# Kernel tuning notes

Measured on AMD Instinct MI355X. Metric: run time of the kernel, lower is better.

Reference implementation:

```python
import jax, jax.numpy as jnp
import numpy as np

B, S, D = 8, 1024, 1024   # batch, routed-over rows, feature dim (input_dim)
E = 1024                  # output_dim (== S so gather indices are in range)
K = 2                     # top-k
ALPHA = 0.01


def setup_inputs() -> dict:
    key = jax.random.key(0)
    kx, kw = jax.random.split(key)
    x = jax.random.normal(kx, (B, S, D), dtype=jnp.float32)
    # nn.Linear(input_dim, output_dim, bias=False) weight: [E, D]
    W = jax.random.normal(kw, (E, D), dtype=jnp.float32) / np.sqrt(D).astype(np.float32)
    return {"x": x, "W": W}


def reference(x, W):
    # logits = proj(x): [B, S, E]  (temperature == 1.0 -> no scaling)
    logits = jnp.einsum('bsd,ed->bse', x, W)
    probs = jax.nn.softmax(logits, axis=-1)
    topk_probs, topk_idx = jax.lax.top_k(probs, K)            # [B, S, K]
    # router_selections: gather rows of x along dim 1 -> [B, S, K, D]
    sel = x[jnp.arange(B)[:, None, None], topk_idx]
    # y = sum_k topk_probs * selected rows -> [B, S, D]
    y = jnp.einsum('bsk,bskd->bsd', topk_probs, sel)
    # auxiliary load-balance loss
    router_probs = probs.mean(axis=(0, 1))                    # [E]
    counts = jnp.bincount(topk_idx.reshape(-1), length=E).astype(probs.dtype)
    router_fraction = counts / counts.sum()
    aux_loss = ALPHA * E * jnp.sum(router_probs * router_fraction)
    return y, aux_loss
```

## Files before the change

kernel.cpp:

```cpp
#include <hip/hip_runtime.h>

#define MTOK 8192
#define ED   1024

typedef short s16x8 __attribute__((ext_vector_type(8)));
typedef float f32x4 __attribute__((ext_vector_type(4)));
typedef unsigned short u16x4 __attribute__((ext_vector_type(4)));

__device__ __forceinline__ unsigned short f2bf(float f) {
    unsigned u = __builtin_bit_cast(unsigned, f);
    u += 0x7fff + ((u >> 16) & 1);
    return (unsigned short)(u >> 16);
}
__device__ __forceinline__ float bf2f(unsigned short h) {
    unsigned u = ((unsigned)h) << 16;
    return __builtin_bit_cast(float, u);
}

__global__ __launch_bounds__(256) void split_bf16_kernel(
        const float* __restrict__ src, unsigned short* __restrict__ hi,
        unsigned short* __restrict__ lo, int n4) {
    int idx = blockIdx.x * 256 + threadIdx.x;
    const int stride = gridDim.x * 256;
    for (; idx < n4; idx += stride) {
        float4 v = ((const float4*)src)[idx];
        u16x4 h, l;
        h[0] = f2bf(v.x); l[0] = f2bf(v.x - bf2f(h[0]));
        h[1] = f2bf(v.y); l[1] = f2bf(v.y - bf2f(h[1]));
        h[2] = f2bf(v.z); l[2] = f2bf(v.z - bf2f(h[2]));
        h[3] = f2bf(v.w); l[3] = f2bf(v.w - bf2f(h[3]));
        ((u16x4*)hi)[idx] = h;
        ((u16x4*)lo)[idx] = l;
    }
}

__device__ __forceinline__ void gload16(const void* g, void* l) {
    __builtin_amdgcn_global_load_lds(
        (const __attribute__((address_space(1))) void*)g,
        (__attribute__((address_space(3))) void*)l, 16, 0, 0);
}

__global__ __launch_bounds__(256, 2) void gemm_mfma_split_kernel(
        const unsigned short* __restrict__ Xhi, const unsigned short* __restrict__ Xlo,
        const unsigned short* __restrict__ Whi, const unsigned short* __restrict__ Wlo,
        float* __restrict__ C) {
    __shared__ unsigned short smem[2 * 16384];

    const int bid = blockIdx.x;
    const int xcd = bid & 7;
    const int j   = bid >> 3;
    const int bm  = xcd * 8 + (j >> 3);
    const int bn  = j & 7;

    const int tid  = threadIdx.x;
    const int lane = tid & 63;
    const int wid  = tid >> 6;

    const int srow = lane >> 2;
    const int sg   = (lane & 3) ^ ((srow >> 1) & 3);
    const unsigned short* gsrc;
    unsigned short* ldst;
    {
        size_t rb;
        if (wid == 0)      { gsrc = Xhi; ldst = smem;         rb = (size_t)bm * 128; }
        else if (wid == 1) { gsrc = Xlo; ldst = smem + 4096;  rb = (size_t)bm * 128; }
        else if (wid == 2) { gsrc = Whi; ldst = smem + 8192;  rb = (size_t)bn * 128; }
        else               { gsrc = Wlo; ldst = smem + 12288; rb = (size_t)bn * 128; }
        gsrc += (rb + srow) * ED + sg * 8;
    }

#define STAGE(buf, kk)                                                        \
    {                                                                          \
        unsigned short* dst = ldst + (buf) * 16384;                            \
        const unsigned short* src = gsrc + (kk);                               \
        _Pragma("unroll")                                                      \
        for (int c = 0; c < 8; ++c)                                            \
            gload16(src + c * (16 * ED), dst + c * 512);                       \
    }

    const int wm = wid >> 1, wn = wid & 1;
    const int fr = lane & 15, fg = lane >> 4;
    const int pg = fg ^ ((fr >> 1) & 3);
    const int aoff = (wm * 64 + fr) * 32 + pg * 8;
    const int boff = (wn * 64 + fr) * 32 + pg * 8;

    f32x4 acc[4][4] = {};

    STAGE(0, 0);
    asm volatile("s_waitcnt vmcnt(0)" ::: "memory");
    __builtin_amdgcn_s_barrier();

    for (int t = 0; t < 32; ++t) {
        const int cur = t & 1;
        if (t < 31) STAGE(cur ^ 1, (t + 1) * 32);

        const unsigned short* Ah = smem + cur * 16384;
        const unsigned short* Al = Ah + 4096;
        const unsigned short* Bh = Ah + 8192;
        const unsigned short* Bl = Ah + 12288;

        s16x8 ah[4], al[4], bh[4], bl[4];
#pragma unroll
        for (int i = 0; i < 4; ++i) {
            ah[i] = *(const s16x8*)&Ah[aoff + i * 512];
            al[i] = *(const s16x8*)&Al[aoff + i * 512];
            bh[i] = *(const s16x8*)&Bh[boff + i * 512];
            bl[i] = *(const s16x8*)&Bl[boff + i * 512];
        }
#pragma unroll
        for (int i = 0; i < 4; ++i)
#pragma unroll
            for (int jj = 0; jj < 4; ++jj) {
                acc[i][jj] = __builtin_amdgcn_mfma_f32_16x16x32_bf16(ah[i], bh[jj], acc[i][jj], 0, 0, 0);
                acc[i][jj] = __builtin_amdgcn_mfma_f32_16x16x32_bf16(ah[i], bl[jj], acc[i][jj], 0, 0, 0);
                acc[i][jj] = __builtin_amdgcn_mfma_f32_16x16x32_bf16(al[i], bh[jj], acc[i][jj], 0, 0, 0);
            }

        asm volatile("s_waitcnt vmcnt(0)" ::: "memory");
        __builtin_amdgcn_s_barrier();
    }
#undef STAGE

    const int crow = bm * 128 + wm * 64 + fg * 4;
    const int ccol = bn * 128 + wn * 64 + fr;
#pragma unroll
    for (int i = 0; i < 4; ++i)
#pragma unroll
        for (int jj = 0; jj < 4; ++jj)
#pragma unroll
            for (int r = 0; r < 4; ++r)
                C[(size_t)(crow + i * 16 + r) * ED + ccol + jj * 16] = acc[i][jj][r];
}

#define BM 128
#define BN 128
#define BK 32
#define LDA (BM + 4)
#define LDB (BN + 4)

__global__ __launch_bounds__(256) void gemm_logits_kernel(const float* __restrict__ X,
                                                          const float* __restrict__ W,
                                                          float* __restrict__ C) {
    __shared__ float As[BK][LDA];
    __shared__ float Bs[BK][LDB];
    const int bm  = blockIdx.y * BM;
    const int bn  = blockIdx.x * BN;
    const int tid = threadIdx.x;
    const int tx  = tid & 15;
    const int ty  = tid >> 4;
    const int lr  = tid >> 3;
    const int lc  = (tid & 7) << 2;

    float acc[8][8];
#pragma unroll
    for (int i = 0; i < 8; ++i)
#pragma unroll
        for (int j = 0; j < 8; ++j) acc[i][j] = 0.f;

    for (int k0 = 0; k0 < ED; k0 += BK) {
#pragma unroll
        for (int i = 0; i < 4; ++i) {
            const int r = lr + i * 32;
            float4 va = *(const float4*)&X[(size_t)(bm + r) * ED + k0 + lc];
            As[lc + 0][r] = va.x; As[lc + 1][r] = va.y;
            As[lc + 2][r] = va.z; As[lc + 3][r] = va.w;
            float4 vb = *(const float4*)&W[(size_t)(bn + r) * ED + k0 + lc];
            Bs[lc + 0][r] = vb.x; Bs[lc + 1][r] = vb.y;
            Bs[lc + 2][r] = vb.z; Bs[lc + 3][r] = vb.w;
        }
        __syncthreads();
#pragma unroll
        for (int kk = 0; kk < BK; ++kk) {
            float a[8], b[8];
            *(float4*)&a[0] = *(const float4*)&As[kk][ty * 8];
            *(float4*)&a[4] = *(const float4*)&As[kk][ty * 8 + 4];
            *(float4*)&b[0] = *(const float4*)&Bs[kk][tx * 8];
            *(float4*)&b[4] = *(const float4*)&Bs[kk][tx * 8 + 4];
#pragma unroll
            for (int i = 0; i < 8; ++i)
#pragma unroll
                for (int j = 0; j < 8; ++j)
                    acc[i][j] = fmaf(a[i], b[j], acc[i][j]);
        }
        __syncthreads();
    }
#pragma unroll
    for (int i = 0; i < 8; ++i) {
        const int r = bm + ty * 8 + i;
        float4* dst = (float4*)&C[(size_t)r * ED + bn + tx * 8];
        dst[0] = make_float4(acc[i][0], acc[i][1], acc[i][2], acc[i][3]);
        dst[1] = make_float4(acc[i][4], acc[i][5], acc[i][6], acc[i][7]);
    }
}

__device__ __forceinline__ bool better(float v, int i, float bv, int bi) {
    return (v > bv) || (v == bv && i < bi);
}

__global__ __launch_bounds__(256, 8) void softmax_wave_kernel(
        const float* __restrict__ X, float* __restrict__ OUT,
        float* __restrict__ partial, int* __restrict__ counts) {
    __shared__ float L[4 * 1024];
    const int tid  = threadIdx.x;
    const int lane = tid & 63;
    const int w    = tid >> 6;
    const int t    = blockIdx.x * 4 + w;

    const float4* row4 = (const float4*)&OUT[(size_t)t * ED];
    float4 p[4];
#pragma unroll
    for (int i = 0; i < 4; ++i) p[i] = row4[lane + 64 * i];

    float v1 = -1e30f, v2 = -1e30f; int i1 = 0x7fffffff, i2 = 0x7fffffff;
#pragma unroll
    for (int i = 0; i < 4; ++i) {
        const float vv[4] = {p[i].x, p[i].y, p[i].z, p[i].w};
#pragma unroll
        for (int c = 0; c < 4; ++c) {
            const int e = 256 * i + 4 * lane + c;
            const float v = vv[c];
            if (better(v, e, v1, i1)) { v2 = v1; i2 = i1; v1 = v; i1 = e; }
            else if (better(v, e, v2, i2)) { v2 = v; i2 = e; }
        }
    }
#pragma unroll
    for (int off = 32; off; off >>= 1) {
        const float ov1 = __shfl_xor(v1, off); const int oi1 = __shfl_xor(i1, off);
        const float ov2 = __shfl_xor(v2, off); const int oi2 = __shfl_xor(i2, off);
        if (better(ov1, oi1, v1, i1)) {
            float nv2; int ni2;
            if (better(v1, i1, ov2, oi2)) { nv2 = v1; ni2 = i1; }
            else { nv2 = ov2; ni2 = oi2; }
            v1 = ov1; i1 = oi1; v2 = nv2; i2 = ni2;
        } else if (better(ov1, oi1, v2, i2)) { v2 = ov1; i2 = oi1; }
    }
    const float m = v1;

    float s = 0.f;
#pragma unroll
    for (int i = 0; i < 4; ++i) {
        p[i].x = __expf(p[i].x - m); p[i].y = __expf(p[i].y - m);
        p[i].z = __expf(p[i].z - m); p[i].w = __expf(p[i].w - m);
        s += p[i].x + p[i].y + p[i].z + p[i].w;
    }
#pragma unroll
    for (int off = 32; off; off >>= 1) s += __shfl_xor(s, off);
    const float inv = 1.f / s;

#pragma unroll
    for (int i = 0; i < 4; ++i) {
        float4 q = make_float4(p[i].x * inv, p[i].y * inv, p[i].z * inv, p[i].w * inv);
        *(float4*)&L[w * 1024 + i * 256 + lane * 4] = q;
    }

    const float p1 = inv;
    const float p2 = __expf(v2 - m) * inv;
    const int b = t >> 10;
    const float4* x1 = (const float4*)&X[((size_t)(b << 10) + i1) * ED];
    const float4* x2 = (const float4*)&X[((size_t)(b << 10) + i2) * ED];
    float4* yrow = (float4*)&OUT[(size_t)t * ED];
#pragma unroll
    for (int i = 0; i < 4; ++i) {
        const int idx = lane + 64 * i;
        const float4 a = x1[idx];
        const float4 c = x2[idx];
        float4 r;
        r.x = fmaf(p1, a.x, p2 * c.x);
        r.y = fmaf(p1, a.y, p2 * c.y);
        r.z = fmaf(p1, a.z, p2 * c.z);
        r.w = fmaf(p1, a.w, p2 * c.w);
        yrow[idx] = r;
    }

    if (lane == 0) { atomicAdd(&counts[i1], 1); atomicAdd(&counts[i2], 1); }

    __syncthreads();
    float4 s0 = *(float4*)&L[0 * 1024 + tid * 4];
    float4 s1 = *(float4*)&L[1 * 1024 + tid * 4];
    float4 s2 = *(float4*)&L[2 * 1024 + tid * 4];
    float4 s3 = *(float4*)&L[3 * 1024 + tid * 4];
    float4 r;
    r.x = (s0.x + s1.x) + (s2.x + s3.x);
    r.y = (s0.y + s1.y) + (s2.y + s3.y);
    r.z = (s0.z + s1.z) + (s2.z + s3.z);
    r.w = (s0.w + s1.w) + (s2.w + s3.w);
    *(float4*)&partial[(size_t)blockIdx.x * 1024 + tid * 4] = r;
}

__global__ __launch_bounds__(256) void aux1_kernel(const float* __restrict__ partial,
                                                   const int* __restrict__ counts,
                                                   float* __restrict__ dotPartial) {
    __shared__ float red[16][16];
    const int tid = threadIdx.x;
    const int el  = tid & 15;
    const int ch  = tid >> 4;
    const int e   = blockIdx.x * 16 + el;
    float s = 0.f;
    for (int k = 0; k < 128; ++k)
        s += partial[(size_t)(ch * 128 + k) * 1024 + e];
    red[ch][el] = s;
    __syncthreads();
    if (tid < 16) {
        float rs = 0.f;
#pragma unroll
        for (int c = 0; c < 16; ++c) rs += red[c][tid];
        float val = rs * (float)counts[blockIdx.x * 16 + tid];
#pragma unroll
        for (int off = 8; off; off >>= 1) val += __shfl_xor(val, off);
        if (tid == 0) dotPartial[blockIdx.x] = val;
    }
}

__global__ void aux2_kernel(const float* __restrict__ dotPartial, float* __restrict__ out) {
    const int lane = threadIdx.x;
    float v = dotPartial[lane];
#pragma unroll
    for (int off = 32; off; off >>= 1) v += __shfl_xor(v, off);
    if (lane == 0)
        out[(size_t)MTOK * ED] = v * (0.01f * 1024.f / (8192.f * 16384.f));
}

#define TOKS_PER_BLK 16
__global__ __launch_bounds__(256) void softmax_topk_y_kernel(
        const float* __restrict__ X, float* __restrict__ OUT,
        float* __restrict__ router_sum, int* __restrict__ counts) {
    __shared__ float routerLocal[ED];
    __shared__ float redMax[4];
    __shared__ float redSum[4];
    __shared__ float wV1[4]; __shared__ int wI1[4];
    __shared__ float wV2[4]; __shared__ int wI2[4];

    const int tid  = threadIdx.x;
    const int lane = tid & 63;
    const int wave = tid >> 6;

    for (int e = tid; e < ED; e += 256) routerLocal[e] = 0.f;
    __syncthreads();

    const int t0 = blockIdx.x * TOKS_PER_BLK;
    for (int t = t0; t < t0 + TOKS_PER_BLK; ++t) {
        const float* lrow = &OUT[(size_t)t * ED];
        float l[4];
#pragma unroll
        for (int i = 0; i < 4; ++i) l[i] = lrow[tid + i * 256];

        float m = fmaxf(fmaxf(l[0], l[1]), fmaxf(l[2], l[3]));
#pragma unroll
        for (int off = 32; off; off >>= 1) m = fmaxf(m, __shfl_xor(m, off));
        if (lane == 0) redMax[wave] = m;
        __syncthreads();
        m = fmaxf(fmaxf(redMax[0], redMax[1]), fmaxf(redMax[2], redMax[3]));

        float p[4]; float s = 0.f;
#pragma unroll
        for (int i = 0; i < 4; ++i) { p[i] = expf(l[i] - m); s += p[i]; }
#pragma unroll
        for (int off = 32; off; off >>= 1) s += __shfl_xor(s, off);
        if (lane == 0) redSum[wave] = s;

        float v1 = -1e30f, v2 = -1e30f; int i1 = 0x7fffffff, i2 = 0x7fffffff;
#pragma unroll
        for (int i = 0; i < 4; ++i) {
            const float v = l[i]; const int ix = tid + i * 256;
            if (better(v, ix, v1, i1)) { v2 = v1; i2 = i1; v1 = v; i1 = ix; }
            else if (better(v, ix, v2, i2)) { v2 = v; i2 = ix; }
        }
#pragma unroll
        for (int off = 32; off; off >>= 1) {
            const float ov1 = __shfl_xor(v1, off); const int oi1 = __shfl_xor(i1, off);
            const float ov2 = __shfl_xor(v2, off); const int oi2 = __shfl_xor(i2, off);
            if (better(ov1, oi1, v1, i1)) {
                float nv2; int ni2;
                if (better(v1, i1, ov2, oi2)) { nv2 = v1; ni2 = i1; }
                else { nv2 = ov2; ni2 = oi2; }
                v1 = ov1; i1 = oi1; v2 = nv2; i2 = ni2;
            } else if (better(ov1, oi1, v2, i2)) { v2 = ov1; i2 = oi1; }
        }
        if (lane == 0) { wV1[wave] = v1; wI1[wave] = i1; wV2[wave] = v2; wI2[wave] = i2; }
        __syncthreads();

        v1 = wV1[0]; i1 = wI1[0]; v2 = wV2[0]; i2 = wI2[0];
#pragma unroll
        for (int w = 1; w < 4; ++w) {
            const float ov1 = wV1[w]; const int oi1 = wI1[w];
            const float ov2 = wV2[w]; const int oi2 = wI2[w];
            if (better(ov1, oi1, v1, i1)) {
                float nv2; int ni2;
                if (better(v1, i1, ov2, oi2)) { nv2 = v1; ni2 = i1; }
                else { nv2 = ov2; ni2 = oi2; }
                v1 = ov1; i1 = oi1; v2 = nv2; i2 = ni2;
            } else if (better(ov1, oi1, v2, i2)) { v2 = ov1; i2 = oi1; }
        }
        const float stot = redSum[0] + redSum[1] + redSum[2] + redSum[3];
        const float inv = 1.f / stot;

#pragma unroll
        for (int i = 0; i < 4; ++i) routerLocal[tid + i * 256] += p[i] * inv;

        const float p1 = expf(v1 - m) * inv;
        const float p2 = expf(v2 - m) * inv;

        const int b = t >> 10;
        const float4* x1 = (const float4*)&X[((size_t)(b << 10) + i1) * ED];
        const float4* x2 = (const float4*)&X[((size_t)(b << 10) + i2) * ED];
        float4* yrow = (float4*)&OUT[(size_t)t * ED];
        const float4 a = x1[tid];
        const float4 c = x2[tid];
        float4 r;
        r.x = fmaf(p1, a.x, p2 * c.x);
        r.y = fmaf(p1, a.y, p2 * c.y);
        r.z = fmaf(p1, a.z, p2 * c.z);
        r.w = fmaf(p1, a.w, p2 * c.w);
        yrow[tid] = r;

        if (tid == 0) { atomicAdd(&counts[i1], 1); atomicAdd(&counts[i2], 1); }
        __syncthreads();
    }

    for (int e = tid; e < ED; e += 256) atomicAdd(&router_sum[e], routerLocal[e]);
}

__global__ __launch_bounds__(256) void aux_kernel(const float* __restrict__ router_sum,
                                                  const int* __restrict__ counts,
                                                  float* __restrict__ out) {
    __shared__ float red[4];
    const int tid = threadIdx.x;
    float s = 0.f;
    for (int e = tid; e < ED; e += 256)
        s += (router_sum[e] * (1.f / 8192.f)) * ((float)counts[e] * (1.f / 16384.f));
#pragma unroll
    for (int off = 32; off; off >>= 1) s += __shfl_xor(s, off);
    if ((tid & 63) == 0) red[tid >> 6] = s;
    __syncthreads();
    if (tid == 0) out[(size_t)MTOK * ED] = 0.01f * 1024.f * (red[0] + red[1] + red[2] + red[3]);
}

extern "C" void kernel_launch(void* const* d_in, const int* in_sizes, int n_in,
                              void* d_out, int out_size, void* d_ws, size_t ws_size,
                              hipStream_t stream) {
    const float* X = (const float*)d_in[0];
    const float* W = (const float*)d_in[1];
    float* out = (float*)d_out;

    const size_t WS_NEED = (size_t)MTOK * ED * 2 * sizeof(unsigned short)
                         + (size_t)ED * ED * 2 * sizeof(unsigned short)
                         + ED * (sizeof(float) + sizeof(int));

    if (ws_size >= WS_NEED) {
        unsigned short* Xhi = (unsigned short*)d_ws;
        unsigned short* Xlo = Xhi + (size_t)MTOK * ED;
        unsigned short* Whi = Xlo + (size_t)MTOK * ED;
        unsigned short* Wlo = Whi + (size_t)ED * ED;
        float* tail         = (float*)(Wlo + (size_t)ED * ED);
        float* dotPartial   = tail;
        int*   counts       = (int*)(tail + ED);
        float* partial      = (float*)Xlo;

        hipMemsetAsync(counts, 0, ED * sizeof(int), stream);
        split_bf16_kernel<<<2048, 256, 0, stream>>>(X, Xhi, Xlo, MTOK * ED / 4);
        split_bf16_kernel<<<512, 256, 0, stream>>>(W, Whi, Wlo, ED * ED / 4);
        gemm_mfma_split_kernel<<<512, 256, 0, stream>>>(Xhi, Xlo, Whi, Wlo, out);
        softmax_wave_kernel<<<MTOK / 4, 256, 0, stream>>>(X, out, partial, counts);
        aux1_kernel<<<64, 256, 0, stream>>>(partial, counts, dotPartial);
        aux2_kernel<<<1, 64, 0, stream>>>(dotPartial, out);
    } else {
        float* router_sum = (float*)d_ws;
        int*   counts     = (int*)((char*)d_ws + ED * sizeof(float));
        hipMemsetAsync(d_ws, 0, ED * (sizeof(float) + sizeof(int)), stream);
        dim3 ggrid(ED / BN, MTOK / BM);
        gemm_logits_kernel<<<ggrid, 256, 0, stream>>>(X, W, out);
        softmax_topk_y_kernel<<<MTOK / TOKS_PER_BLK, 256, 0, stream>>>(X, out, router_sum, counts);
        aux_kernel<<<1, 256, 0, stream>>>(router_sum, counts, out);
    }
}
```

Measured before the change: 101.2 us.

## Software-pipeline GEMM main loop with register double-buffered LDS fragments

Restructures the split-bf16 GEMM K-loop into a two-stage unrolled pipeline. Fragments for the next tile are read from LDS into a second register set while the MFMAs for the current tile run, and global-to-LDS prefetch stays two tiles deep using partial vmcnt waits instead of draining to zero every iteration. The aim is to hide LDS and global latency behind MFMA work. The cost is doubled fragment registers, which may lower occupancy, and more complex barrier and waitcnt ordering.

```diff
diff --git a/kernel.cpp b/kernel.cpp
--- a/kernel.cpp
+++ b/kernel.cpp
@@ -84,42 +84,62 @@
     const int aoff = (wm * 64 + fr) * 32 + pg * 8;
     const int boff = (wn * 64 + fr) * 32 + pg * 8;
 
+    s16x8 ah0[4], al0[4], bh0[4], bl0[4];
+    s16x8 ah1[4], al1[4], bh1[4], bl1[4];
     f32x4 acc[4][4] = {};
 
+#define READF(S, BUF)                                                         \
+    {                                                                          \
+        const unsigned short* _b = smem + (BUF) * 16384;                       \
+        _Pragma("unroll")                                                      \
+        for (int i = 0; i < 4; ++i) {                                          \
+            ah##S[i] = *(const s16x8*)&_b[aoff + i * 512];                     \
+            al##S[i] = *(const s16x8*)&_b[4096 + aoff + i * 512];              \
+            bh##S[i] = *(const s16x8*)&_b[8192 + boff + i * 512];              \
+            bl##S[i] = *(const s16x8*)&_b[12288 + boff + i * 512];             \
+        }                                                                      \
+    }
+
+#define MFMAC(S)                                                               \
+    _Pragma("unroll")                                                          \
+    for (int i = 0; i < 4; ++i)                                                \
+        _Pragma("unroll")                                                      \
+        for (int jj = 0; jj < 4; ++jj) {                                       \
+            acc[i][jj] = __builtin_amdgcn_mfma_f32_16x16x32_bf16(ah##S[i], bh##S[jj], acc[i][jj], 0, 0, 0); \
+            acc[i][jj] = __builtin_amdgcn_mfma_f32_16x16x32_bf16(ah##S[i], bl##S[jj], acc[i][jj], 0, 0, 0); \
+            acc[i][jj] = __builtin_amdgcn_mfma_f32_16x16x32_bf16(al##S[i], bh##S[jj], acc[i][jj], 0, 0, 0); \
+        }
+
     STAGE(0, 0);
+    STAGE(1, 32);
+    asm volatile("s_waitcnt vmcnt(8)" ::: "memory");
+    __builtin_amdgcn_s_barrier();
+    READF(0, 0);
+
+    for (int t2 = 0; t2 < 30; t2 += 2) {
+        asm volatile("s_waitcnt lgkmcnt(0)" ::: "memory");
+        __builtin_amdgcn_s_barrier();
+        STAGE(0, (t2 + 2) * 32);
+        asm volatile("s_waitcnt vmcnt(8)" ::: "memory");
+        __builtin_amdgcn_s_barrier();
+        READF(1, 1);
+        MFMAC(0);
+        asm volatile("s_waitcnt lgkmcnt(0)" ::: "memory");
+        __builtin_amdgcn_s_barrier();
+        STAGE(1, (t2 + 3) * 32);
+        asm volatile("s_waitcnt vmcnt(8)" ::: "memory");
+        __builtin_amdgcn_s_barrier();
+        READF(0, 0);
+        MFMAC(1);
+    }
     asm volatile("s_waitcnt vmcnt(0)" ::: "memory");
     __builtin_amdgcn_s_barrier();
-
-    for (int t = 0; t < 32; ++t) {
-        const int cur = t & 1;
-        if (t < 31) STAGE(cur ^ 1, (t + 1) * 32);
-
-        const unsigned short* Ah = smem + cur * 16384;
-        const unsigned short* Al = Ah + 4096;
-        const unsigned short* Bh = Ah + 8192;
-        const unsigned short* Bl = Ah + 12288;
-
-        s16x8 ah[4], al[4], bh[4], bl[4];
-#pragma unroll
-        for (int i = 0; i < 4; ++i) {
-            ah[i] = *(const s16x8*)&Ah[aoff + i * 512];
-            al[i] = *(const s16x8*)&Al[aoff + i * 512];
-            bh[i] = *(const s16x8*)&Bh[boff + i * 512];
-            bl[i] = *(const s16x8*)&Bl[boff + i * 512];
-        }
-#pragma unroll
-        for (int i = 0; i < 4; ++i)
-#pragma unroll
-            for (int jj = 0; jj < 4; ++jj) {
-                acc[i][jj] = __builtin_amdgcn_mfma_f32_16x16x32_bf16(ah[i], bh[jj], acc[i][jj], 0, 0, 0);
-                acc[i][jj] = __builtin_amdgcn_mfma_f32_16x16x32_bf16(ah[i], bl[jj], acc[i][jj], 0, 0, 0);
-                acc[i][jj] = __builtin_amdgcn_mfma_f32_16x16x32_bf16(al[i], bh[jj], acc[i][jj], 0, 0, 0);
-            }
-
-        asm volatile("s_waitcnt vmcnt(0)" ::: "memory");
-        __builtin_amdgcn_s_barrier();
-    }
+    READF(1, 1);
+    MFMAC(0);
+    MFMAC(1);
 #undef STAGE
+#undef READF
+#undef MFMAC
 
     const int crow = bm * 128 + wm * 64 + fg * 4;
     const int ccol = bn * 128 + wn * 64 + fr;
```

Result: no change. 100.9 us (-0.3%).

## Fuse X bf16 hi/lo split into GEMM by loading fp32 tiles to LDS

Applied to the files above, without the earlier changes.

Removes the separate pass that splits X (8192x1024 fp32) into bf16 hi/lo arrays. The GEMM now stages fp32 X tiles into LDS with a swizzle and converts them to hi/lo bf16 in registers using v_cvt_pk_bf16_f32 before the MFMAs. This drops a full read and write of the X split buffers and shrinks the workspace. In exchange it doubles the LDS footprint per buffer, moves conversion ALU work into the GEMM inner loop, and adds an lgkmcnt wait. The conversion is redone by each of the 8 column blocks that reads a given X tile.

```diff
diff --git a/kernel.cpp b/kernel.cpp
--- a/kernel.cpp
+++ b/kernel.cpp
@@ -5,6 +5,7 @@
 
 typedef short s16x8 __attribute__((ext_vector_type(8)));
 typedef float f32x4 __attribute__((ext_vector_type(4)));
+typedef int   i32x4 __attribute__((ext_vector_type(4)));
 typedef unsigned short u16x4 __attribute__((ext_vector_type(4)));
 
 __device__ __forceinline__ unsigned short f2bf(float f) {
@@ -40,11 +41,17 @@
         (__attribute__((address_space(3))) void*)l, 16, 0, 0);
 }
 
+__device__ __forceinline__ int cvtpk(float a, float b) {
+    int r;
+    asm("v_cvt_pk_bf16_f32 %0, %1, %2" : "=v"(r) : "v"(a), "v"(b));
+    return r;
+}
+
 __global__ __launch_bounds__(256, 2) void gemm_mfma_split_kernel(
-        const unsigned short* __restrict__ Xhi, const unsigned short* __restrict__ Xlo,
+        const float* __restrict__ Xf,
         const unsigned short* __restrict__ Whi, const unsigned short* __restrict__ Wlo,
         float* __restrict__ C) {
-    __shared__ unsigned short smem[2 * 16384];
+    __shared__ __align__(16) unsigned char smem[2 * 32768];
 
     const int bid = blockIdx.x;
     const int xcd = bid & 7;
@@ -56,33 +63,33 @@
     const int lane = tid & 63;
     const int wid  = tid >> 6;
 
+    const float* gsrcF = Xf + (size_t)(bm * 128 + wid * 64 + (lane >> 3)) * ED
+                            + (((lane & 7) ^ (lane >> 3)) << 2);
     const int srow = lane >> 2;
     const int sg   = (lane & 3) ^ ((srow >> 1) & 3);
-    const unsigned short* gsrc;
-    unsigned short* ldst;
-    {
-        size_t rb;
-        if (wid == 0)      { gsrc = Xhi; ldst = smem;         rb = (size_t)bm * 128; }
-        else if (wid == 1) { gsrc = Xlo; ldst = smem + 4096;  rb = (size_t)bm * 128; }
-        else if (wid == 2) { gsrc = Whi; ldst = smem + 8192;  rb = (size_t)bn * 128; }
-        else               { gsrc = Wlo; ldst = smem + 12288; rb = (size_t)bn * 128; }
-        gsrc += (rb + srow) * ED + sg * 8;
-    }
-
-#define STAGE(buf, kk)                                                        \
-    {                                                                          \
-        unsigned short* dst = ldst + (buf) * 16384;                            \
-        const unsigned short* src = gsrc + (kk);                               \
-        _Pragma("unroll")                                                      \
-        for (int c = 0; c < 8; ++c)                                            \
-            gload16(src + c * (16 * ED), dst + c * 512);                       \
+    const unsigned short* gsrcS =
+        ((wid == 3) ? Wlo : Whi) + (size_t)(bn * 128 + srow) * ED + sg * 8;
+    unsigned char* const dstU = smem + ((wid < 2) ? wid * 8192
+                                                  : 16384 + (wid - 2) * 8192);
+
+#define STAGE(buf, kk)                                                          \
+    if (wid < 2) {                                                              \
+        _Pragma("unroll")                                                       \
+        for (int c = 0; c < 8; ++c)                                             \
+            gload16(gsrcF + (kk) + c * (8 * ED), dstU + (buf) * 32768 + c * 1024); \
+    } else {                                                                    \
+        _Pragma("unroll")                                                       \
+        for (int c = 0; c < 8; ++c)                                             \
+            gload16(gsrcS + (kk) + c * (16 * ED), dstU + (buf) * 32768 + c * 1024); \
     }
 
     const int wm = wid >> 1, wn = wid & 1;
     const int fr = lane & 15, fg = lane >> 4;
     const int pg = fg ^ ((fr >> 1) & 3);
-    const int aoff = (wm * 64 + fr) * 32 + pg * 8;
-    const int boff = (wn * 64 + fr) * 32 + pg * 8;
+    const int boff = ((wn * 64 + fr) * 32 + pg * 8) * 2;
+    const int aswz = fr & 7;
+    const int slot0 = (2 * fg) ^ aswz;
+    const int slot1 = slot0 ^ 1;
 
     f32x4 acc[4][4] = {};
 
@@ -94,18 +101,32 @@
         const int cur = t & 1;
         if (t < 31) STAGE(cur ^ 1, (t + 1) * 32);
 
-        const unsigned short* Ah = smem + cur * 16384;
-        const unsigned short* Al = Ah + 4096;
-        const unsigned short* Bh = Ah + 8192;
-        const unsigned short* Bl = Ah + 12288;
+        const unsigned char* bufb = smem + cur * 32768;
+        const float4* Af4 = (const float4*)bufb;
 
         s16x8 ah[4], al[4], bh[4], bl[4];
 #pragma unroll
         for (int i = 0; i < 4; ++i) {
-            ah[i] = *(const s16x8*)&Ah[aoff + i * 512];
-            al[i] = *(const s16x8*)&Al[aoff + i * 512];
-            bh[i] = *(const s16x8*)&Bh[boff + i * 512];
-            bl[i] = *(const s16x8*)&Bl[boff + i * 512];
+            const int rowb = (wm * 64 + i * 16 + fr) * 8;
+            const float4 f0 = Af4[rowb + slot0];
+            const float4 f1 = Af4[rowb + slot1];
+            i32x4 h, l;
+            h[0] = cvtpk(f0.x, f0.y);
+            h[1] = cvtpk(f0.z, f0.w);
+            h[2] = cvtpk(f1.x, f1.y);
+            h[3] = cvtpk(f1.z, f1.w);
+            l[0] = cvtpk(f0.x - __builtin_bit_cast(float, h[0] << 16),
+                         f0.y - __builtin_bit_cast(float, h[0] & 0xffff0000));
+            l[1] = cvtpk(f0.z - __builtin_bit_cast(float, h[1] << 16),
+                         f0.w - __builtin_bit_cast(float, h[1] & 0xffff0000));
+            l[2] = cvtpk(f1.x - __builtin_bit_cast(float, h[2] << 16),
+                         f1.y - __builtin_bit_cast(float, h[2] & 0xffff0000));
+            l[3] = cvtpk(f1.z - __builtin_bit_cast(float, h[3] << 16),
+                         f1.w - __builtin_bit_cast(float, h[3] & 0xffff0000));
+            ah[i] = __builtin_bit_cast(s16x8, h);
+            al[i] = __builtin_bit_cast(s16x8, l);
+            bh[i] = *(const s16x8*)(bufb + 16384 + boff + i * 1024);
+            bl[i] = *(const s16x8*)(bufb + 24576 + boff + i * 1024);
         }
 #pragma unroll
         for (int i = 0; i < 4; ++i)
@@ -116,7 +137,7 @@
                 acc[i][jj] = __builtin_amdgcn_mfma_f32_16x16x32_bf16(al[i], bh[jj], acc[i][jj], 0, 0, 0);
             }
 
-        asm volatile("s_waitcnt vmcnt(0)" ::: "memory");
+        asm volatile("s_waitcnt vmcnt(0) lgkmcnt(0)" ::: "memory");
         __builtin_amdgcn_s_barrier();
     }
 #undef STAGE
@@ -442,24 +463,20 @@
     const float* W = (const float*)d_in[1];
     float* out = (float*)d_out;
 
-    const size_t WS_NEED = (size_t)MTOK * ED * 2 * sizeof(unsigned short)
-                         + (size_t)ED * ED * 2 * sizeof(unsigned short)
-                         + ED * (sizeof(float) + sizeof(int));
+    const size_t WS_NEED = (size_t)ED * ED * 2 * sizeof(unsigned short)
+                         + (size_t)2048 * 1024 * sizeof(float)
+                         + 64 * sizeof(float) + ED * sizeof(int);
 
     if (ws_size >= WS_NEED) {
-        unsigned short* Xhi = (unsigned short*)d_ws;
-        unsigned short* Xlo = Xhi + (size_t)MTOK * ED;
-        unsigned short* Whi = Xlo + (size_t)MTOK * ED;
+        unsigned short* Whi = (unsigned short*)d_ws;
         unsigned short* Wlo = Whi + (size_t)ED * ED;
-        float* tail         = (float*)(Wlo + (size_t)ED * ED);
-        float* dotPartial   = tail;
-        int*   counts       = (int*)(tail + ED);
-        float* partial      = (float*)Xlo;
+        float* partial      = (float*)(Wlo + (size_t)ED * ED);
+        float* dotPartial   = partial + (size_t)2048 * 1024;
+        int*   counts       = (int*)(dotPartial + 64);
 
         hipMemsetAsync(counts, 0, ED * sizeof(int), stream);
-        split_bf16_kernel<<<2048, 256, 0, stream>>>(X, Xhi, Xlo, MTOK * ED / 4);
         split_bf16_kernel<<<512, 256, 0, stream>>>(W, Whi, Wlo, ED * ED / 4);
-        gemm_mfma_split_kernel<<<512, 256, 0, stream>>>(Xhi, Xlo, Whi, Wlo, out);
+        gemm_mfma_split_kernel<<<512, 256, 0, stream>>>(X, Whi, Wlo, out);
         softmax_wave_kernel<<<MTOK / 4, 256, 0, stream>>>(X, out, partial, counts);
         aux1_kernel<<<64, 256, 0, stream>>>(partial, counts, dotPartial);
         aux2_kernel<<<1, 64, 0, stream>>>(dotPartial, out);
```

New measurement: 95.06 us. 6.1% less time.
